# Kernel tuning notes

Measured on AMD Instinct MI355X. Metric: run time of the kernel, lower is better.

The kernel has to match this reference:

```python
import jax, jax.numpy as jnp
import numpy as np

B, N, F_DIM, M, K, D = 8, 16384, 6, 128, 16, 768
MLP_DIMS = [F_DIM, 256, 512, 768, D]


def _fps(pts):
    """Deterministic farthest point sampling. pts: [N,4] -> indices [M] (first pick = point 0)."""
    n = pts.shape[0]

    def step(carry, _):
        min_d, last = carry
        d = jnp.sum((pts - pts[last]) ** 2, axis=-1)
        min_d = jnp.minimum(min_d, d)
        nxt = jnp.argmax(min_d).astype(jnp.int32)
        return (min_d, nxt), nxt

    init = (jnp.full((n,), 1e30, dtype=pts.dtype), jnp.int32(0))
    _, idx = jax.lax.scan(step, init, None, length=M - 1)
    return jnp.concatenate([jnp.zeros((1,), jnp.int32), idx])


def setup_inputs() -> dict:
    key = jax.random.key(0)
    ks = jax.random.split(key, 16)
    bidx = jnp.repeat(jnp.arange(B, dtype=jnp.float32), N)[:, None]
    xyzt = jax.random.normal(ks[0], (B * N, 4), jnp.float32)
    coordinates = jnp.concatenate([bidx, xyzt], axis=1)  # [B*N, 5]
    features = jax.random.normal(ks[1], (B * N, F_DIM), jnp.float32)
    inp = {"coordinates": coordinates, "features": features}
    for i in range(4):
        di, do = MLP_DIMS[i], MLP_DIMS[i + 1]
        inp[f"W{i}"] = jax.random.normal(ks[2 + i], (di, do), jnp.float32) * np.float32(1.0 / np.sqrt(di))
        inp[f"b{i}"] = jnp.zeros((do,), jnp.float32)
    for j in range(2):
        inp[f"Wn{j}"] = jax.random.normal(ks[6 + j], (D, D), jnp.float32) * np.float32(1.0 / np.sqrt(D))
        inp[f"bn{j}"] = jnp.zeros((D,), jnp.float32)
    return inp


def _forward(coordinates, features, W0, b0, W1, b1, W2, b2, W3, b3, Wn0, bn0, Wn1, bn1):
    # Equal points per event, sorted batch ids -> plain reshape replaces the per-batch loop.
    pts = coordinates.reshape(B, N, 5)[:, :, 1:5]       # xyz + time  [B,N,4]
    h = features.reshape(B, N, F_DIM)
    # per-point MLP (ReLU after each hidden layer, final Linear has no activation)
    h = jax.nn.relu(h @ W0 + b0)
    h = jax.nn.relu(h @ W1 + b1)
    h = jax.nn.relu(h @ W2 + b2)
    pf = h @ W3 + b3                                    # [B,N,D]
    # FPS centroids (non-differentiable index selection, as in the torch/cpu original)
    fidx = jax.vmap(_fps)(jax.lax.stop_gradient(pts))   # [B,M]
    cent = jnp.take_along_axis(pts, fidx[:, :, None], axis=1)  # [B,M,4]
    # cdist + kNN (smallest distances)
    dist = jnp.sqrt(jnp.sum((cent[:, :, None, :] - pts[:, None, :, :]) ** 2, axis=-1))  # [B,M,N]
    _, knn = jax.lax.top_k(-dist, K)                    # [B,M,K]
    gathered = jax.vmap(lambda p, i: p[i])(pf, knn)     # [B,M,K,D]
    pooled = jnp.max(gathered, axis=2)                  # [B,M,D]
    t = jax.nn.relu(pooled @ Wn0 + bn0)
    tokens = t @ Wn1 + bn1                              # [B,M,D]
    # sort tokens/centroids by centroid time (column 3)
    order = jnp.argsort(cent[:, :, 3], axis=1)
    cent = jnp.take_along_axis(cent, order[:, :, None], axis=1)
    tokens = jnp.take_along_axis(tokens, order[:, :, None], axis=1)
    masks = jnp.ones((B, M), dtype=bool)  # num_points > max_tokens -> all tokens valid
    return tokens, cent, masks


def reference(coordinates, features, W0, b0, W1, b1, W2, b2, W3, b3, Wn0, bn0, Wn1, bn1):
    return _forward(coordinates, features, W0, b0, W1, b1, W2, b2, W3, b3, Wn0, bn0, Wn1, bn1)
```

## Files before the change

### kernel.cpp

```cpp
#include <hip/hip_runtime.h>

#define B_ 8
#define N_ 16384
#define F_ 6
#define M_ 128
#define K_ 16
#define D_ 768

typedef unsigned short u16;
typedef unsigned int u32;
typedef unsigned long long u64;
typedef __attribute__((ext_vector_type(8))) short short8;
typedef __attribute__((ext_vector_type(4))) float f32x4;
typedef __attribute__((ext_vector_type(2))) float f32x2;

__device__ __forceinline__ u16 f2bf(float f){
  union { float f; u32 i; } v; v.f = f;
  u32 x = v.i;
  u32 r = x + 0x7FFFu + ((x >> 16) & 1u);
  return (u16)(r >> 16);
}

__device__ __forceinline__ void ld_g2l(const u16* g, u16* l){
  __builtin_amdgcn_global_load_lds((const __attribute__((address_space(1))) u32*)g,
                                   (__attribute__((address_space(3))) u32*)l, 16, 0, 0);
}

__device__ __forceinline__ f32x4 ld_x4(const float* p){
  f32x4 r;
  asm volatile("global_load_dwordx4 %0, %1, off" : "=v"(r) : "v"(p) : "memory");
  return r;
}

template<int CTRL>
__device__ __forceinline__ float dppmax(float v){
  union { float f; int i; } a, r;
  a.f = v;
  r.i = __builtin_amdgcn_update_dpp(a.i, a.i, CTRL, 0xF, 0xF, false);
  return fmaxf(v, r.f);
}
template<int CTRL>
__device__ __forceinline__ float dppmin(float v){
  union { float f; int i; } a, r;
  a.f = v;
  r.i = __builtin_amdgcn_update_dpp(a.i, a.i, CTRL, 0xF, 0xF, false);
  return fminf(v, r.f);
}
template<int CTRL>
__device__ __forceinline__ int dppimin(int v){
  int r = __builtin_amdgcn_update_dpp(v, v, CTRL, 0xF, 0xF, false);
  return (r < v) ? r : v;
}

#define FPT 32
__global__ __launch_bounds__(512)
void fps_conv(const float* __restrict__ coords,
              float* __restrict__ cent_sorted,
              float* __restrict__ out, size_t out_elems,
              const float* __restrict__ W1, const float* __restrict__ W2,
              const float* __restrict__ W3, const float* __restrict__ Wn0,
              const float* __restrict__ Wn1, u16* __restrict__ Wb){
#pragma clang fp contract(off)
  __shared__ u16 tile[64][65];
  __shared__ f32x4 carr[M_];
  __shared__ float swv[2][8];
  __shared__ int   swi[2][8];
  int blk = blockIdx.x;
  int t = threadIdx.x;

  if (blk >= 8){
    int cblk = blk - 8;
    const float* W; u16* WT; int K, N, lb;
    if      (cblk < 32)  { W = W1;  WT = Wb;           K = 256; N = 512; lb = cblk; }
    else if (cblk < 128) { W = W2;  WT = Wb + 131072;  K = 512; N = 768; lb = cblk - 32; }
    else if (cblk < 272) { W = W3;  WT = Wb + 524288;  K = 768; N = 768; lb = cblk - 128; }
    else if (cblk < 416) { W = Wn0; WT = Wb + 1114112; K = 768; N = 768; lb = cblk - 272; }
    else                 { W = Wn1; WT = Wb + 1703936; K = 768; N = 768; lb = cblk - 416; }
    int tiles_n = N >> 6;
    int tk = lb / tiles_n, tn = lb % tiles_n;
    int k0 = tk << 6, n0 = tn << 6;
#pragma unroll
    for (int q = 0; q < 8; q++){
      int idx = q * 512 + t;
      int kk = idx >> 6, nn = idx & 63;
      tile[kk][nn] = f2bf(W[(size_t)(k0 + kk) * N + n0 + nn]);
    }
    __syncthreads();
#pragma unroll
    for (int q = 0; q < 8; q++){
      int idx = q * 512 + t;
      int nn = idx >> 6, kk = idx & 63;
      WT[(size_t)(n0 + nn) * K + k0 + kk] = tile[kk][nn];
    }
    return;
  }

  int b = blk;
  int lane = t & 63, wave = t >> 6;
  const float* cb = coords + (size_t)b * N_ * 5;
  const int base = t << 5;
  f32x4 p[FPT];
#pragma unroll
  for (int k = 0; k < FPT; k++){
    p[k] = ld_x4(cb + (size_t)(base + k) * 5 + 1);
  }
  float md[FPT];
#pragma unroll
  for (int k = 0; k < FPT; k++) md[k] = 1e30f;
  asm volatile("s_waitcnt vmcnt(0)" ::: "memory");
  __builtin_amdgcn_sched_barrier(0);
  float cx = cb[1], cy = cb[2], cz = cb[3], ct = cb[4];
  if (t == 0) carr[0] = (f32x4){cx, cy, cz, ct};
  for (int step = 1; step < M_; step++){
    float bv = -1.0f; int bl = 0;
#pragma unroll
    for (int k = 0; k < FPT; k++){
      f32x2 xy = (f32x2){p[k][0], p[k][1]};
      f32x2 zw = (f32x2){p[k][2], p[k][3]};
      float dx = xy[0] - cx;
      float dy = xy[1] - cy;
      float dz = zw[0] - cz;
      float dw = zw[1] - ct;
      float s = ((dx*dx + dy*dy) + dz*dz) + dw*dw;
      float m = fminf(s, md[k]);
      md[k] = m;
      if (m > bv){ bv = m; bl = k; }
    }
    int bi = base + bl;
    float r = bv;
    r = dppmax<0x111>(r);
    r = dppmax<0x112>(r);
    r = dppmax<0x114>(r);
    r = dppmax<0x118>(r);
    r = dppmax<0x142>(r);
    r = dppmax<0x143>(r);
    union { float f; int i; } rm; rm.f = r;
    union { int i; float f; } wmu; wmu.i = __builtin_amdgcn_readlane(rm.i, 63);
    float wmax = wmu.f;
    u64 wmask = __ballot(bv == wmax);
    int srcL = (int)__ffsll((unsigned long long)wmask) - 1;
    int wbi = __builtin_amdgcn_readlane(bi, srcL);
    int par = step & 1;
    if (lane == 0){ swv[par][wave] = wmax; swi[par][wave] = wbi; }
    __syncthreads();
    float fv = swv[par][0]; int fi = swi[par][0];
#pragma unroll
    for (int w = 1; w < 8; w++){
      float v = swv[par][w];
      int  iw = swi[par][w];
      if (v > fv){ fv = v; fi = iw; }
    }
    int widx = __builtin_amdgcn_readfirstlane(fi);
    size_t wb = (size_t)widx * 5;
    cx = cb[wb+1]; cy = cb[wb+2]; cz = cb[wb+3]; ct = cb[wb+4];
    if (t == 0) carr[step] = (f32x4){cx, cy, cz, ct};
  }
  __syncthreads();
  if (t < M_){
    f32x4 row = carr[t];
    float w = row[3];
    int rank = 0;
    for (int j = 0; j < M_; j++){
      float tj = carr[j][3];
      if (tj < w || (tj == w && j < t)) rank++;
    }
    float* dst = cent_sorted + ((size_t)b * M_ + rank) * 4;
    dst[0]=row[0]; dst[1]=row[1]; dst[2]=row[2]; dst[3]=w;
    size_t co = (size_t)B_ * M_ * D_ + ((size_t)b * M_ + rank) * 4;
    if (co + 3 < out_elems){
      out[co+0]=row[0]; out[co+1]=row[1]; out[co+2]=row[2]; out[co+3]=w;
    }
    size_t mo = (size_t)B_ * M_ * D_ + (size_t)B_ * M_ * 4 + (size_t)b * M_ + t;
    if (mo < out_elems) out[mo] = 1.0f;
  }
}

#define KNT 512
#define KPT 32
__global__ __launch_bounds__(512) void knn_kernel(const float* __restrict__ coords,
                                                  const float* __restrict__ cent,
                                                  int* __restrict__ knn){
#pragma clang fp contract(off)
  int cm = blockIdx.x;
  int b = cm >> 7;
  const float* cb = coords + (size_t)b * N_ * 5;
  int t = threadIdx.x;
  float cx=cent[cm*4+0], cy=cent[cm*4+1], cz=cent[cm*4+2], ct=cent[cm*4+3];
  float dist[KPT];
#pragma unroll
  for (int j = 0; j < KPT; j++){
    size_t i = t + j * KNT;
    float dx=cb[i*5+1]-cx, dy=cb[i*5+2]-cy, dz=cb[i*5+3]-cz, dw=cb[i*5+4]-ct;
    float d = ((dx*dx + dy*dy) + dz*dz) + dw*dw;
    dist[j] = sqrtf(d);
  }
  __shared__ float s_wv[8];
  __shared__ int s_wi[8];
  __shared__ int s_bi;
  for (int r = 0; r < K_; r++){
    float bv = 3e38f; int bi = 1 << 30;
#pragma unroll
    for (int j = 0; j < KPT; j++){
      int i = t + j * KNT;
      float v = dist[j];
      if (v < bv){ bv = v; bi = i; }
    }
    float rv = bv;
    rv = dppmin<0x111>(rv);
    rv = dppmin<0x112>(rv);
    rv = dppmin<0x114>(rv);
    rv = dppmin<0x118>(rv);
    rv = dppmin<0x142>(rv);
    rv = dppmin<0x143>(rv);
    union { float f; int i; } rmu; rmu.f = rv;
    union { int i; float f; } wmn; wmn.i = __builtin_amdgcn_readlane(rmu.i, 63);
    float wmin = wmn.f;
    int cand = (bv == wmin) ? bi : 0x7FFFFFFF;
    cand = dppimin<0x111>(cand);
    cand = dppimin<0x112>(cand);
    cand = dppimin<0x114>(cand);
    cand = dppimin<0x118>(cand);
    cand = dppimin<0x142>(cand);
    cand = dppimin<0x143>(cand);
    int wbi = __builtin_amdgcn_readlane(cand, 63);
    if ((t & 63) == 0){ s_wv[t >> 6] = wmin; s_wi[t >> 6] = wbi; }
    __syncthreads();
    if (t == 0){
      float fv = s_wv[0]; int fi = s_wi[0];
      for (int w = 1; w < 8; w++){
        float wv = s_wv[w]; int wi = s_wi[w];
        if (wv < fv || (wv == fv && wi < fi)){ fv = wv; fi = wi; }
      }
      s_bi = fi;
      knn[(size_t)cm * K_ + r] = fi & (N_ - 1);
    }
    __syncthreads();
    int wi = s_bi;
#pragma unroll
    for (int j = 0; j < KPT; j++){
      if (t + j * KNT == wi) dist[j] = 3e38f;
    }
  }
}

__global__ __launch_bounds__(256) void gather_l0(const float* __restrict__ feat,
                                                 const int* __restrict__ knn,
                                                 const float* __restrict__ W0,
                                                 const float* __restrict__ b0,
                                                 u16* __restrict__ h1,
                                                 int rowBase){
  __shared__ float sW[F_][256];
  __shared__ float sb[256];
  __shared__ float sfa[32][F_];
  int t = threadIdx.x;
#pragma unroll
  for (int k = 0; k < F_; k++) sW[k][t] = W0[k * 256 + t];
  sb[t] = b0[t];
  if (t < 32 * F_){
    int r = t / F_, k = t % F_;
    int grow = rowBase + blockIdx.x * 32 + r;
    int bb = grow >> 11;
    int idx = knn[grow] & (N_ - 1);
    sfa[r][k] = feat[((size_t)bb * N_ + idx) * F_ + k];
  }
  __syncthreads();
#pragma unroll 4
  for (int r = 0; r < 32; r++){
    float acc = sb[t];
#pragma unroll
    for (int k = 0; k < F_; k++) acc = fmaf(sfa[r][k], sW[k][t], acc);
    int lrow = blockIdx.x * 32 + r;
    h1[(size_t)lrow * 256 + t] = f2bf(fmaxf(acc, 0.0f));
  }
}

template<int RELU, int OUTF32>
__global__ __launch_bounds__(256) void gemm_bf16(const u16* __restrict__ A,
                                                 const u16* __restrict__ WT,
                                                 const float* __restrict__ bias,
                                                 void* __restrict__ Cv,
                                                 int Kd, int Nd){
  __shared__ u16 As[128][32];
  __shared__ u16 Bs[128][32];
  const int t = threadIdx.x;
  const int bm = blockIdx.y << 7;
  const int bn = blockIdx.x << 7;
  const int wave = t >> 6;
  const int lane = t & 63;
  const int wm = (wave & 1) << 6;
  const int wn = (wave >> 1) << 6;
  const int lm = lane & 15;
  const int lk = (lane >> 4) << 3;
  u16* AsF = &As[0][0];
  u16* BsF = &Bs[0][0];
  const int wbase = wave << 6;
  f32x4 acc[4][4] = {};
  for (int k0 = 0; k0 < Kd; k0 += 32){
#pragma unroll
    for (int it = 0; it < 2; it++){
      int slot = t + (it << 8);
      int r = slot >> 2;
      int c = (slot & 3) << 3;
      int dst = (wbase + (it << 8)) << 3;
      ld_g2l(A  + (size_t)(bm + r) * Kd + k0 + c, AsF + dst);
      ld_g2l(WT + (size_t)(bn + r) * Kd + k0 + c, BsF + dst);
    }
    __syncthreads();
    short8 af[4], bfr[4];
#pragma unroll
    for (int mt = 0; mt < 4; mt++) af[mt] = *(const short8*)&As[wm + (mt << 4) + lm][lk];
#pragma unroll
    for (int nt = 0; nt < 4; nt++) bfr[nt] = *(const short8*)&Bs[wn + (nt << 4) + lm][lk];
#pragma unroll
    for (int mt = 0; mt < 4; mt++)
#pragma unroll
      for (int nt = 0; nt < 4; nt++)
        acc[mt][nt] = __builtin_amdgcn_mfma_f32_16x16x32_bf16(af[mt], bfr[nt], acc[mt][nt], 0, 0, 0);
    __syncthreads();
  }
#pragma unroll
  for (int nt = 0; nt < 4; nt++){
    int n = bn + wn + (nt << 4) + lm;
    float bia = bias[n];
#pragma unroll
    for (int mt = 0; mt < 4; mt++){
#pragma unroll
      for (int r2 = 0; r2 < 4; r2++){
        int m = bm + wm + (mt << 4) + ((lane >> 4) << 2) + r2;
        float v = acc[mt][nt][r2] + bia;
        if (RELU) v = fmaxf(v, 0.0f);
        if (OUTF32) ((float*)Cv)[(size_t)m * Nd + n] = v;
        else        ((u16*)Cv)[(size_t)m * Nd + n] = f2bf(v);
      }
    }
  }
}

template<int RELU, int OUTF32>
__global__ __launch_bounds__(256) void gemm64(const u16* __restrict__ A,
                                              const u16* __restrict__ WT,
                                              const float* __restrict__ bias,
                                              void* __restrict__ Cv,
                                              int Kd, int Nd){
  __shared__ u16 As[64][32];
  __shared__ u16 Bs[64][32];
  const int t = threadIdx.x;
  const int bm = blockIdx.y << 6;
  const int bn = blockIdx.x << 6;
  const int wave = t >> 6;
  const int lane = t & 63;
  const int wm = (wave & 1) << 5;
  const int wn = (wave >> 1) << 5;
  const int lm = lane & 15;
  const int lk = (lane >> 4) << 3;
  u16* AsF = &As[0][0];
  u16* BsF = &Bs[0][0];
  const int wbase = wave << 6;
  f32x4 acc[2][2] = {};
  for (int k0 = 0; k0 < Kd; k0 += 32){
    {
      int r = t >> 2;
      int c = (t & 3) << 3;
      int dst = wbase << 3;
      ld_g2l(A  + (size_t)(bm + r) * Kd + k0 + c, AsF + dst);
      ld_g2l(WT + (size_t)(bn + r) * Kd + k0 + c, BsF + dst);
    }
    __syncthreads();
    short8 af[2], bfr[2];
#pragma unroll
    for (int mt = 0; mt < 2; mt++) af[mt] = *(const short8*)&As[wm + (mt << 4) + lm][lk];
#pragma unroll
    for (int nt = 0; nt < 2; nt++) bfr[nt] = *(const short8*)&Bs[wn + (nt << 4) + lm][lk];
#pragma unroll
    for (int mt = 0; mt < 2; mt++)
#pragma unroll
      for (int nt = 0; nt < 2; nt++)
        acc[mt][nt] = __builtin_amdgcn_mfma_f32_16x16x32_bf16(af[mt], bfr[nt], acc[mt][nt], 0, 0, 0);
    __syncthreads();
  }
#pragma unroll
  for (int nt = 0; nt < 2; nt++){
    int n = bn + wn + (nt << 4) + lm;
    float bia = bias[n];
#pragma unroll
    for (int mt = 0; mt < 2; mt++){
#pragma unroll
      for (int r2 = 0; r2 < 4; r2++){
        int m = bm + wm + (mt << 4) + ((lane >> 4) << 2) + r2;
        float v = acc[mt][nt][r2] + bia;
        if (RELU) v = fmaxf(v, 0.0f);
        if (OUTF32) ((float*)Cv)[(size_t)m * Nd + n] = v;
        else        ((u16*)Cv)[(size_t)m * Nd + n] = f2bf(v);
      }
    }
  }
}

__global__ __launch_bounds__(256) void gemm_pool(const u16* __restrict__ A,
                                                 const u16* __restrict__ WT,
                                                 const float* __restrict__ bias,
                                                 u16* __restrict__ pooled,
                                                 int Kd, int Nd, int groupBase){
  __shared__ u16 As[128][32];
  __shared__ u16 Bs[128][32];
  const int t = threadIdx.x;
  const int bm = blockIdx.y << 7;
  const int bn = blockIdx.x << 7;
  const int wave = t >> 6;
  const int lane = t & 63;
  const int wm = (wave & 1) << 6;
  const int wn = (wave >> 1) << 6;
  const int lm = lane & 15;
  const int lk = (lane >> 4) << 3;
  u16* AsF = &As[0][0];
  u16* BsF = &Bs[0][0];
  const int wbase = wave << 6;
  f32x4 acc[4][4] = {};
  for (int k0 = 0; k0 < Kd; k0 += 32){
#pragma unroll
    for (int it = 0; it < 2; it++){
      int slot = t + (it << 8);
      int r = slot >> 2;
      int c = (slot & 3) << 3;
      int dst = (wbase + (it << 8)) << 3;
      ld_g2l(A  + (size_t)(bm + r) * Kd + k0 + c, AsF + dst);
      ld_g2l(WT + (size_t)(bn + r) * Kd + k0 + c, BsF + dst);
    }
    __syncthreads();
    short8 af[4], bfr[4];
#pragma unroll
    for (int mt = 0; mt < 4; mt++) af[mt] = *(const short8*)&As[wm + (mt << 4) + lm][lk];
#pragma unroll
    for (int nt = 0; nt < 4; nt++) bfr[nt] = *(const short8*)&Bs[wn + (nt << 4) + lm][lk];
#pragma unroll
    for (int mt = 0; mt < 4; mt++)
#pragma unroll
      for (int nt = 0; nt < 4; nt++)
        acc[mt][nt] = __builtin_amdgcn_mfma_f32_16x16x32_bf16(af[mt], bfr[nt], acc[mt][nt], 0, 0, 0);
    __syncthreads();
  }
#pragma unroll
  for (int nt = 0; nt < 4; nt++){
    int n = bn + wn + (nt << 4) + lm;
    float bia = bias[n];
#pragma unroll
    for (int mt = 0; mt < 4; mt++){
      f32x4 a = acc[mt][nt];
      float v = fmaxf(fmaxf(a[0], a[1]), fmaxf(a[2], a[3]));
      v = fmaxf(v, __shfl_xor(v, 16));
      v = fmaxf(v, __shfl_xor(v, 32));
      if ((lane >> 4) == 0){
        int g = groupBase + (bm >> 4) + (wm >> 4) + mt;
        pooled[(size_t)g * Nd + n] = f2bf(v + bia);
      }
    }
  }
}

__global__ __launch_bounds__(256) void fill_diag(float* __restrict__ out, size_t out_elems){
  size_t i = (size_t)blockIdx.x * 256 + threadIdx.x;
  if (i >= out_elems) return;
  size_t maskStart = (size_t)B_ * M_ * D_ + (size_t)B_ * M_ * 4;
  out[i] = (i >= maskStart) ? 1.0f : 0.0f;
}

extern "C" void kernel_launch(void* const* d_in, const int* in_sizes, int n_in,
                              void* d_out, int out_size, void* d_ws, size_t ws_size,
                              hipStream_t stream){
  (void)in_sizes; (void)n_in;
  const float* coords   = (const float*)d_in[0];
  const float* features = (const float*)d_in[1];
  const float* W0 = (const float*)d_in[2];  const float* b0 = (const float*)d_in[3];
  const float* W1 = (const float*)d_in[4];  const float* b1 = (const float*)d_in[5];
  const float* W2 = (const float*)d_in[6];  const float* b2 = (const float*)d_in[7];
  const float* W3 = (const float*)d_in[8];  const float* b3 = (const float*)d_in[9];
  const float* Wn0 = (const float*)d_in[10]; const float* bn0 = (const float*)d_in[11];
  const float* Wn1 = (const float*)d_in[12]; const float* bn1 = (const float*)d_in[13];
  float* out = (float*)d_out;
  const size_t out_elems = (size_t)out_size;

  char* ws = (char*)d_ws;
  const size_t o_cent = 0;
  const size_t o_cntS = 16384;
  const size_t o_knn  = 32768;
  const size_t o_Wb   = 131072;
  const size_t o_pool = 4718592;
  const size_t o_t1   = 6291456;
  const size_t o_chunk= 7864320;
  const int ROWS = B_ * M_ * K_;
  (void)o_cent;

  int R = 16384;
  while (R > 128 && o_chunk + (size_t)R * 2560 > ws_size) R >>= 1;
  if (d_ws == nullptr || o_chunk + (size_t)R * 2560 > ws_size){
    fill_diag<<<(int)((out_elems + 255) / 256), 256, 0, stream>>>(out, out_elems);
    return;
  }

  float* cent_sorted = (float*)(ws + o_cntS);
  int*   knn         = (int*)(ws + o_knn);
  u16* Wb   = (u16*)(ws + o_Wb);
  u16* W1t  = Wb;               u16* W2t  = Wb + 131072;
  u16* W3t  = Wb + 524288;      u16* Wn0t = Wb + 1114112;
  u16* Wn1t = Wb + 1703936;
  u16* pooled = (u16*)(ws + o_pool);
  u16* t1     = (u16*)(ws + o_t1);
  u16* regA   = (u16*)(ws + o_chunk);
  u16* regB   = (u16*)(ws + o_chunk + (size_t)R * 1536);

  fps_conv<<<568, 512, 0, stream>>>(coords, cent_sorted, out, out_elems,
                                    W1, W2, W3, Wn0, Wn1, Wb);
  knn_kernel<<<B_ * M_, KNT, 0, stream>>>(coords, cent_sorted, knn);

  for (int rowBase = 0; rowBase < ROWS; rowBase += R){
    gather_l0<<<R / 32, 256, 0, stream>>>(features, knn, W0, b0, regA, rowBase);
    gemm_bf16<1,0><<<dim3(4, R / 128), 256, 0, stream>>>(regA, W1t, b1, regB, 256, 512);
    gemm_bf16<1,0><<<dim3(6, R / 128), 256, 0, stream>>>(regB, W2t, b2, regA, 512, 768);
    gemm_pool<<<dim3(6, R / 128), 256, 0, stream>>>(regA, W3t, b3, pooled, 768, 768, rowBase >> 4);
  }

  gemm64<1,0><<<dim3(12, (B_ * M_) / 64), 256, 0, stream>>>(pooled, Wn0t, bn0, t1, 768, 768);
  gemm64<0,1><<<dim3(12, (B_ * M_) / 64), 256, 0, stream>>>(t1, Wn1t, bn1, out, 768, 768);
}
```

Measured before the change: 498.0 us.

## Overlap kNN with FPS by streaming centroids through tagged global flags

The separate kNN kernel is folded into the FPS kernel as 248 extra worker blocks. Each FPS block publishes every centroid as it is chosen, using tagged 64-bit atomic stores, and the workers spin-wait on those tags so each centroid's kNN search runs while FPS is still going. Because centroids are now handled in FPS order rather than time-sorted order, an inverse permutation is written and gather_l0 indexes the kNN results through it. This relies on all blocks being co-resident, since spinning workers could otherwise deadlock, and it adds a zeroing kernel plus spin-wait polling.

```diff
diff --git a/kernel.cpp b/kernel.cpp
--- a/kernel.cpp
+++ b/kernel.cpp
@@ -52,23 +52,43 @@
   return (r < v) ? r : v;
 }
 
+__device__ __forceinline__ void pub_cent(u64* pb, int m, float x, float y, float z, float w){
+  union { float f; u32 u; } c0, c1, c2, c3;
+  c0.f = x; c1.f = y; c2.f = z; c3.f = w;
+  u64 tag = ((u64)(u32)(m + 1)) << 32;
+  __hip_atomic_store(pb + 0, tag | c0.u, __ATOMIC_RELAXED, __HIP_MEMORY_SCOPE_AGENT);
+  __hip_atomic_store(pb + 1, tag | c1.u, __ATOMIC_RELAXED, __HIP_MEMORY_SCOPE_AGENT);
+  __hip_atomic_store(pb + 2, tag | c2.u, __ATOMIC_RELAXED, __HIP_MEMORY_SCOPE_AGENT);
+  __hip_atomic_store(pb + 3, tag | c3.u, __ATOMIC_RELAXED, __HIP_MEMORY_SCOPE_AGENT);
+}
+
+__global__ __launch_bounds__(256) void zero_pub(u64* __restrict__ pub){
+  pub[(size_t)blockIdx.x * 256 + threadIdx.x] = 0ull;
+}
+
 #define FPT 32
+#define KNW 248
+#define KNT 512
+#define KPT 32
 __global__ __launch_bounds__(512)
 void fps_conv(const float* __restrict__ coords,
-              float* __restrict__ cent_sorted,
               float* __restrict__ out, size_t out_elems,
               const float* __restrict__ W1, const float* __restrict__ W2,
               const float* __restrict__ W3, const float* __restrict__ Wn0,
-              const float* __restrict__ Wn1, u16* __restrict__ Wb){
+              const float* __restrict__ Wn1, u16* __restrict__ Wb,
+              u64* __restrict__ cpub, int* __restrict__ invp,
+              int* __restrict__ knn_fps){
 #pragma clang fp contract(off)
   __shared__ u16 tile[64][65];
   __shared__ f32x4 carr[M_];
   __shared__ float swv[2][8];
   __shared__ int   swi[2][8];
+  __shared__ int   s_bi;
+  __shared__ f32x4 scent;
   int blk = blockIdx.x;
   int t = threadIdx.x;
 
-  if (blk >= 8){
+  if (blk >= 8 && blk < 568){
     int cblk = blk - 8;
     const float* W; u16* WT; int K, N, lb;
     if      (cblk < 32)  { W = W1;  WT = Wb;           K = 256; N = 512; lb = cblk; }
@@ -95,6 +115,78 @@
     return;
   }
 
+  if (blk >= 568){
+    int w = blk - 568;
+    for (int p = w; p < B_ * M_; p += KNW){
+      int m = p >> 3, b = p & 7;
+      if (t == 0){
+        const u64* pb = cpub + (((size_t)b << 7) + m) * 4;
+        u32 want = (u32)(m + 1);
+        u64 v0, v1, v2, v3;
+        for (;;){
+          v0 = __hip_atomic_load(pb + 0, __ATOMIC_RELAXED, __HIP_MEMORY_SCOPE_AGENT);
+          v1 = __hip_atomic_load(pb + 1, __ATOMIC_RELAXED, __HIP_MEMORY_SCOPE_AGENT);
+          v2 = __hip_atomic_load(pb + 2, __ATOMIC_RELAXED, __HIP_MEMORY_SCOPE_AGENT);
+          v3 = __hip_atomic_load(pb + 3, __ATOMIC_RELAXED, __HIP_MEMORY_SCOPE_AGENT);
+          if ((u32)(v0 >> 32) == want && (u32)(v1 >> 32) == want &&
+              (u32)(v2 >> 32) == want && (u32)(v3 >> 32) == want) break;
+          __builtin_amdgcn_s_sleep(2);
+        }
+        union { u32 u; float f; } d0, d1, d2, d3;
+        d0.u = (u32)v0; d1.u = (u32)v1; d2.u = (u32)v2; d3.u = (u32)v3;
+        scent = (f32x4){d0.f, d1.f, d2.f, d3.f};
+      }
+      __syncthreads();
+      float cx = scent[0], cy = scent[1], cz = scent[2], ct = scent[3];
+      const float* cb = coords + (size_t)b * N_ * 5;
+      float dist[KPT];
+#pragma unroll
+      for (int j = 0; j < KPT; j++){
+        size_t i = t + j * KNT;
+        float dx=cb[i*5+1]-cx, dy=cb[i*5+2]-cy, dz=cb[i*5+3]-cz, dw=cb[i*5+4]-ct;
+        float d = ((dx*dx + dy*dy) + dz*dz) + dw*dw;
+        dist[j] = sqrtf(d);
+      }
+      for (int r = 0; r < K_; r++){
+        float bv = 3e38f; int bi = 1 << 30;
+#pragma unroll
+        for (int j = 0; j < KPT; j++){
+          int i = t + j * KNT;
+          float v = dist[j];
+          if (v < bv){ bv = v; bi = i; }
+        }
+        float rv = bv;
+        rv = dppmin<0x111>(rv); rv = dppmin<0x112>(rv); rv = dppmin<0x114>(rv);
+        rv = dppmin<0x118>(rv); rv = dppmin<0x142>(rv); rv = dppmin<0x143>(rv);
+        union { float f; int i; } rmu; rmu.f = rv;
+        union { int i; float f; } wmn; wmn.i = __builtin_amdgcn_readlane(rmu.i, 63);
+        float wmin = wmn.f;
+        int cand = (bv == wmin) ? bi : 0x7FFFFFFF;
+        cand = dppimin<0x111>(cand); cand = dppimin<0x112>(cand); cand = dppimin<0x114>(cand);
+        cand = dppimin<0x118>(cand); cand = dppimin<0x142>(cand); cand = dppimin<0x143>(cand);
+        int wbi = __builtin_amdgcn_readlane(cand, 63);
+        if ((t & 63) == 0){ swv[0][t >> 6] = wmin; swi[0][t >> 6] = wbi; }
+        __syncthreads();
+        if (t == 0){
+          float fv = swv[0][0]; int fi = swi[0][0];
+          for (int ww = 1; ww < 8; ww++){
+            float wv = swv[0][ww]; int wi = swi[0][ww];
+            if (wv < fv || (wv == fv && wi < fi)){ fv = wv; fi = wi; }
+          }
+          s_bi = fi;
+          knn_fps[(((size_t)b << 7) + m) * K_ + r] = fi & (N_ - 1);
+        }
+        __syncthreads();
+        int wi = s_bi;
+#pragma unroll
+        for (int j = 0; j < KPT; j++){
+          if (t + j * KNT == wi) dist[j] = 3e38f;
+        }
+      }
+    }
+    return;
+  }
+
   int b = blk;
   int lane = t & 63, wave = t >> 6;
   const float* cb = coords + (size_t)b * N_ * 5;
@@ -110,17 +202,18 @@
   asm volatile("s_waitcnt vmcnt(0)" ::: "memory");
   __builtin_amdgcn_sched_barrier(0);
   float cx = cb[1], cy = cb[2], cz = cb[3], ct = cb[4];
-  if (t == 0) carr[0] = (f32x4){cx, cy, cz, ct};
+  if (t == 0){
+    carr[0] = (f32x4){cx, cy, cz, ct};
+    pub_cent(cpub + ((size_t)b << 7) * 4, 0, cx, cy, cz, ct);
+  }
   for (int step = 1; step < M_; step++){
     float bv = -1.0f; int bl = 0;
 #pragma unroll
     for (int k = 0; k < FPT; k++){
-      f32x2 xy = (f32x2){p[k][0], p[k][1]};
-      f32x2 zw = (f32x2){p[k][2], p[k][3]};
-      float dx = xy[0] - cx;
-      float dy = xy[1] - cy;
-      float dz = zw[0] - cz;
-      float dw = zw[1] - ct;
+      float dx = p[k][0] - cx;
+      float dy = p[k][1] - cy;
+      float dz = p[k][2] - cz;
+      float dw = p[k][3] - ct;
       float s = ((dx*dx + dy*dy) + dz*dz) + dw*dw;
       float m = fminf(s, md[k]);
       md[k] = m;
@@ -128,12 +221,8 @@
     }
     int bi = base + bl;
     float r = bv;
-    r = dppmax<0x111>(r);
-    r = dppmax<0x112>(r);
-    r = dppmax<0x114>(r);
-    r = dppmax<0x118>(r);
-    r = dppmax<0x142>(r);
-    r = dppmax<0x143>(r);
+    r = dppmax<0x111>(r); r = dppmax<0x112>(r); r = dppmax<0x114>(r);
+    r = dppmax<0x118>(r); r = dppmax<0x142>(r); r = dppmax<0x143>(r);
     union { float f; int i; } rm; rm.f = r;
     union { int i; float f; } wmu; wmu.i = __builtin_amdgcn_readlane(rm.i, 63);
     float wmax = wmu.f;
@@ -153,7 +242,10 @@
     int widx = __builtin_amdgcn_readfirstlane(fi);
     size_t wb = (size_t)widx * 5;
     cx = cb[wb+1]; cy = cb[wb+2]; cz = cb[wb+3]; ct = cb[wb+4];
-    if (t == 0) carr[step] = (f32x4){cx, cy, cz, ct};
+    if (t == 0){
+      carr[step] = (f32x4){cx, cy, cz, ct};
+      pub_cent(cpub + (((size_t)b << 7) + step) * 4, step, cx, cy, cz, ct);
+    }
   }
   __syncthreads();
   if (t < M_){
@@ -164,8 +256,7 @@
       float tj = carr[j][3];
       if (tj < w || (tj == w && j < t)) rank++;
     }
-    float* dst = cent_sorted + ((size_t)b * M_ + rank) * 4;
-    dst[0]=row[0]; dst[1]=row[1]; dst[2]=row[2]; dst[3]=w;
+    invp[(b << 7) + rank] = t;
     size_t co = (size_t)B_ * M_ * D_ + ((size_t)b * M_ + rank) * 4;
     if (co + 3 < out_elems){
       out[co+0]=row[0]; out[co+1]=row[1]; out[co+2]=row[2]; out[co+3]=w;
@@ -175,76 +266,9 @@
   }
 }
 
-#define KNT 512
-#define KPT 32
-__global__ __launch_bounds__(512) void knn_kernel(const float* __restrict__ coords,
-                                                  const float* __restrict__ cent,
-                                                  int* __restrict__ knn){
-#pragma clang fp contract(off)
-  int cm = blockIdx.x;
-  int b = cm >> 7;
-  const float* cb = coords + (size_t)b * N_ * 5;
-  int t = threadIdx.x;
-  float cx=cent[cm*4+0], cy=cent[cm*4+1], cz=cent[cm*4+2], ct=cent[cm*4+3];
-  float dist[KPT];
-#pragma unroll
-  for (int j = 0; j < KPT; j++){
-    size_t i = t + j * KNT;
-    float dx=cb[i*5+1]-cx, dy=cb[i*5+2]-cy, dz=cb[i*5+3]-cz, dw=cb[i*5+4]-ct;
-    float d = ((dx*dx + dy*dy) + dz*dz) + dw*dw;
-    dist[j] = sqrtf(d);
-  }
-  __shared__ float s_wv[8];
-  __shared__ int s_wi[8];
-  __shared__ int s_bi;
-  for (int r = 0; r < K_; r++){
-    float bv = 3e38f; int bi = 1 << 30;
-#pragma unroll
-    for (int j = 0; j < KPT; j++){
-      int i = t + j * KNT;
-      float v = dist[j];
-      if (v < bv){ bv = v; bi = i; }
-    }
-    float rv = bv;
-    rv = dppmin<0x111>(rv);
-    rv = dppmin<0x112>(rv);
-    rv = dppmin<0x114>(rv);
-    rv = dppmin<0x118>(rv);
-    rv = dppmin<0x142>(rv);
-    rv = dppmin<0x143>(rv);
-    union { float f; int i; } rmu; rmu.f = rv;
-    union { int i; float f; } wmn; wmn.i = __builtin_amdgcn_readlane(rmu.i, 63);
-    float wmin = wmn.f;
-    int cand = (bv == wmin) ? bi : 0x7FFFFFFF;
-    cand = dppimin<0x111>(cand);
-    cand = dppimin<0x112>(cand);
-    cand = dppimin<0x114>(cand);
-    cand = dppimin<0x118>(cand);
-    cand = dppimin<0x142>(cand);
-    cand = dppimin<0x143>(cand);
-    int wbi = __builtin_amdgcn_readlane(cand, 63);
-    if ((t & 63) == 0){ s_wv[t >> 6] = wmin; s_wi[t >> 6] = wbi; }
-    __syncthreads();
-    if (t == 0){
-      float fv = s_wv[0]; int fi = s_wi[0];
-      for (int w = 1; w < 8; w++){
-        float wv = s_wv[w]; int wi = s_wi[w];
-        if (wv < fv || (wv == fv && wi < fi)){ fv = wv; fi = wi; }
-      }
-      s_bi = fi;
-      knn[(size_t)cm * K_ + r] = fi & (N_ - 1);
-    }
-    __syncthreads();
-    int wi = s_bi;
-#pragma unroll
-    for (int j = 0; j < KPT; j++){
-      if (t + j * KNT == wi) dist[j] = 3e38f;
-    }
-  }
-}
-
 __global__ __launch_bounds__(256) void gather_l0(const float* __restrict__ feat,
                                                  const int* __restrict__ knn,
+                                                 const int* __restrict__ invp,
                                                  const float* __restrict__ W0,
                                                  const float* __restrict__ b0,
                                                  u16* __restrict__ h1,
@@ -260,7 +284,10 @@
     int r = t / F_, k = t % F_;
     int grow = rowBase + blockIdx.x * 32 + r;
     int bb = grow >> 11;
-    int idx = knn[grow] & (N_ - 1);
+    int ms = (grow >> 4) & 127;
+    int kk = grow & 15;
+    int mf = invp[(bb << 7) + ms];
+    int idx = knn[((((size_t)bb << 7) + mf) << 4) + kk] & (N_ - 1);
     sfa[r][k] = feat[((size_t)bb * N_ + idx) * F_ + k];
   }
   __syncthreads();
@@ -480,15 +507,15 @@
   const size_t out_elems = (size_t)out_size;
 
   char* ws = (char*)d_ws;
-  const size_t o_cent = 0;
-  const size_t o_cntS = 16384;
+  const size_t o_pub  = 0;
   const size_t o_knn  = 32768;
+  const size_t o_invp = 98304;
   const size_t o_Wb   = 131072;
   const size_t o_pool = 4718592;
   const size_t o_t1   = 6291456;
   const size_t o_chunk= 7864320;
   const int ROWS = B_ * M_ * K_;
-  (void)o_cent;
+  (void)o_pub;
 
   int R = 16384;
   while (R > 128 && o_chunk + (size_t)R * 2560 > ws_size) R >>= 1;
@@ -497,8 +524,9 @@
     return;
   }
 
-  float* cent_sorted = (float*)(ws + o_cntS);
-  int*   knn         = (int*)(ws + o_knn);
+  u64* cpub = (u64*)(ws + o_pub);
+  int* knnb = (int*)(ws + o_knn);
+  int* invp = (int*)(ws + o_invp);
   u16* Wb   = (u16*)(ws + o_Wb);
   u16* W1t  = Wb;               u16* W2t  = Wb + 131072;
   u16* W3t  = Wb + 524288;      u16* Wn0t = Wb + 1114112;
@@ -508,12 +536,13 @@
   u16* regA   = (u16*)(ws + o_chunk);
   u16* regB   = (u16*)(ws + o_chunk + (size_t)R * 1536);
 
-  fps_conv<<<568, 512, 0, stream>>>(coords, cent_sorted, out, out_elems,
-                                    W1, W2, W3, Wn0, Wn1, Wb);
-  knn_kernel<<<B_ * M_, KNT, 0, stream>>>(coords, cent_sorted, knn);
+  zero_pub<<<16, 256, 0, stream>>>(cpub);
+  fps_conv<<<816, 512, 0, stream>>>(coords, out, out_elems,
+                                    W1, W2, W3, Wn0, Wn1, Wb,
+                                    cpub, invp, knnb);
 
   for (int rowBase = 0; rowBase < ROWS; rowBase += R){
-    gather_l0<<<R / 32, 256, 0, stream>>>(features, knn, W0, b0, regA, rowBase);
+    gather_l0<<<R / 32, 256, 0, stream>>>(features, knnb, invp, W0, b0, regA, rowBase);
     gemm_bf16<1,0><<<dim3(4, R / 128), 256, 0, stream>>>(regA, W1t, b1, regB, 256, 512);
     gemm_bf16<1,0><<<dim3(6, R / 128), 256, 0, stream>>>(regB, W2t, b2, regA, 512, 768);
     gemm_pool<<<dim3(6, R / 128), 256, 0, stream>>>(regA, W3t, b3, pooled, 768, 768, rowBase >> 4);
```

Result: no change. 502.5 us (+0.9%).
